# Optimization experiments

Hardware: AMD Instinct MI355X
Metric: run time of the kernel (lower is better)

Reference implementation:

```python
import jax, jax.numpy as jnp
import numpy as np

B, A, C, M, E = 8, 100000, 8, 128, 32
ALPHA, GAMMA = 0.25, 2.0


def setup_inputs() -> dict:
    key = jax.random.key(0)
    k1, k2, k3, k4, k5, k6, k7 = jax.random.split(key, 7)
    classifications = jax.random.uniform(k1, (B, A, C), dtype=jnp.float32)
    regressions = jax.random.normal(k2, (B, A, 8), dtype=jnp.float32)
    embeddings = jax.random.normal(k3, (B, A, E), dtype=jnp.float32)
    # anchors: random centers on a 1920x1080 image, reasonable w/h -> x1,y1,x2,y2
    cx = jax.random.uniform(k4, (A,), minval=0.0, maxval=1920.0)
    cy = jax.random.uniform(jax.random.fold_in(k4, 1), (A,), minval=0.0, maxval=1080.0)
    w = jax.random.uniform(jax.random.fold_in(k4, 2), (A,), minval=16.0, maxval=256.0)
    h = jax.random.uniform(jax.random.fold_in(k4, 3), (A,), minval=16.0, maxval=256.0)
    anchors = jnp.stack([cx - 0.5 * w, cy - 0.5 * h, cx + 0.5 * w, cy + 0.5 * h], axis=1)[None].astype(jnp.float32)
    # annotations: 16 coords = jittered 3D-box corner projections around a random box,
    # col 16 = object id, col 17 = class label in [0, C)
    bcx = jax.random.uniform(k5, (B, M, 1), minval=100.0, maxval=1820.0)
    bcy = jax.random.uniform(jax.random.fold_in(k5, 1), (B, M, 1), minval=100.0, maxval=980.0)
    bw = jax.random.uniform(jax.random.fold_in(k5, 2), (B, M, 1), minval=30.0, maxval=300.0)
    bh = jax.random.uniform(jax.random.fold_in(k5, 3), (B, M, 1), minval=30.0, maxval=300.0)
    jit = jax.random.uniform(k6, (B, M, 16), minval=-0.4, maxval=0.4)
    sx = jnp.array([-1, -1, 1, 1, -1, -1, 1, 1], jnp.float32)
    sy = jnp.array([-1, 1, -1, 1, -1, 1, -1, 1], jnp.float32)
    xs = bcx + 0.5 * bw * (sx + jit[..., 0:16:2])
    ys = bcy + 0.5 * bh * (sy + jit[..., 1:16:2])
    coords = jnp.stack([xs, ys], axis=-1).reshape(B, M, 16)
    ids = jax.random.randint(k7, (B, M, 1), 0, 1000).astype(jnp.float32)
    cls_lab = jax.random.randint(jax.random.fold_in(k7, 1), (B, M, 1), 0, C).astype(jnp.float32)
    annotations = jnp.concatenate([coords, ids, cls_lab], axis=-1)
    return {
        "classifications": classifications,
        "regressions": regressions,
        "anchors": anchors,
        "annotations": annotations,
        "embeddings": embeddings,
    }


def calc_iou(a, b):
    # a: [A,4], b: [M,4] in x1,y1,x2,y2 -> [A,M]
    area = (b[:, 2] - b[:, 0]) * (b[:, 3] - b[:, 1])
    iw = jnp.minimum(a[:, 2:3], b[None, :, 2]) - jnp.maximum(a[:, 0:1], b[None, :, 0])
    ih = jnp.minimum(a[:, 3:4], b[None, :, 3]) - jnp.maximum(a[:, 1:2], b[None, :, 1])
    iw = jnp.clip(iw, 0.0)
    ih = jnp.clip(ih, 0.0)
    ua = ((a[:, 2] - a[:, 0]) * (a[:, 3] - a[:, 1]))[:, None] + area[None, :] - iw * ih
    return iw * ih / jnp.clip(ua, 1e-8)


_S2 = jnp.array([-1, -1, 1, 1, -1, -1, 1, 1], jnp.float32)
_S4 = jnp.array([-1, 1, -1, 1, -1, 1, -1, 1], jnp.float32)
_S6 = jnp.array([1, 1, 1, 1, -1, -1, -1, -1], jnp.float32)


def _per_image(cls, reg, ann, anchor):
    # cls [A,C], reg [A,8], ann [M,18], anchor [A,4]
    aw = anchor[:, 2] - anchor[:, 0]
    ah = anchor[:, 3] - anchor[:, 1]
    acx = anchor[:, 0] + 0.5 * aw
    acy = anchor[:, 1] + 0.5 * ah
    cls = jnp.clip(cls, 1e-4, 1.0 - 1e-4)
    valid = ann[:, -1] >= 0.0  # [M]; annotations with class -1 are padding
    xs, ys = ann[:, 0:16:2], ann[:, 1:16:2]
    box2d = jnp.stack([xs.min(1), ys.min(1), xs.max(1), ys.max(1)], axis=1)  # [M,4]
    iou = jnp.where(valid[None, :], calc_iou(anchor, box2d), -1.0)  # [A,M]
    iou_max = iou.max(1)
    assigned = ann[iou.argmax(1)]  # [A,18]
    pos = iou_max >= 0.5
    neg = iou_max < 0.4
    num_pos = jnp.maximum(pos.sum().astype(cls.dtype), 1.0)

    onehot = jax.nn.one_hot(assigned[:, -1].astype(jnp.int32), cls.shape[1], dtype=cls.dtype)
    targets = jnp.where(pos[:, None], onehot, jnp.where(neg[:, None], 0.0, -1.0))
    alpha_f = jnp.where(targets == 1.0, ALPHA, 1.0 - ALPHA)
    focal_w = alpha_f * jnp.where(targets == 1.0, 1.0 - cls, cls) ** GAMMA
    bce = -(targets * jnp.log(cls) + (1.0 - targets) * jnp.log(1.0 - cls))
    cls_loss = jnp.where(targets != -1.0, focal_w * bce, 0.0).sum() / num_pos

    t = assigned[:, :16]

    def vp(rx, ry, tx, ty):
        denom = jnp.sqrt(rx * rx + ry * ry) * jnp.sqrt(tx * tx + ty * ty)
        return 1.0 - (rx * tx + ry * ty) / jnp.maximum(denom, 1e-8)

    vp1 = vp(reg[:, 2], reg[:, 3],
             (t[:, 4] + t[:, 6] + t[:, 12] + t[:, 14] - (t[:, 0] + t[:, 2] + t[:, 8] + t[:, 10])) / 4.0,
             (t[:, 5] + t[:, 7] + t[:, 13] + t[:, 15] - (t[:, 1] + t[:, 3] + t[:, 9] + t[:, 11])) / 4.0)
    vp2 = vp(reg[:, 4], reg[:, 5],
             (t[:, 2] + t[:, 6] + t[:, 10] + t[:, 14] - (t[:, 0] + t[:, 4] + t[:, 8] + t[:, 12])) / 4.0,
             (t[:, 3] + t[:, 7] + t[:, 11] + t[:, 15] - (t[:, 1] + t[:, 5] + t[:, 9] + t[:, 13])) / 4.0)
    vp3 = vp(reg[:, 6], reg[:, 7],
             (t[:, 0] + t[:, 2] + t[:, 4] + t[:, 6] - (t[:, 8] + t[:, 10] + t[:, 12] + t[:, 14])) / 4.0,
             (t[:, 1] + t[:, 3] + t[:, 5] + t[:, 7] - (t[:, 9] + t[:, 11] + t[:, 13] + t[:, 15])) / 4.0)
    vp_all = (vp1 + vp2 + vp3) / 3.0
    vp_loss = (vp_all * pos).sum() / num_pos

    # corner predictions from (ctr_x, ctr_y, v1, v2, v3) offsets: [A,8] x-coords, [A,8] y-coords
    px = reg[:, 0:1] + reg[:, 2:3] * _S2 + reg[:, 4:5] * _S4 + reg[:, 6:7] * _S6
    py = reg[:, 1:2] + reg[:, 3:4] * _S2 + reg[:, 5:6] * _S4 + reg[:, 7:8] * _S6
    tx = (t[:, 0:16:2] - acx[:, None]) / aw[:, None]
    ty = (t[:, 1:16:2] - acy[:, None]) / ah[:, None]
    diff = jnp.concatenate([jnp.abs(px - tx), jnp.abs(py - ty)], axis=1)  # [A,16]
    sl1 = jnp.where(diff <= 1.0 / 9.0, 0.5 * 9.0 * diff * diff, diff - 0.5 / 9.0)
    reg_loss = (sl1.mean(1) * pos).sum() / num_pos
    return cls_loss, reg_loss, vp_loss


def reference(classifications, regressions, anchors, annotations, embeddings):
    anchor = anchors[0]
    cls_l, reg_l, vp_l = jax.vmap(_per_image, in_axes=(0, 0, 0, None))(
        classifications, regressions, annotations, anchor)
    return jnp.stack([cls_l.mean(), reg_l.mean(), vp_l.mean()])


if __name__ == "__main__":
    print(reference(**setup_inputs()))
```

## Files before the change

kernel.cpp:

```cpp
#include <hip/hip_runtime.h>

namespace {

constexpr int B_N = 8;
constexpr int A_N = 100000;
constexpr int M_N = 128;
constexpr int BLOCK = 256;
constexpr int NBLK_S = (A_N + BLOCK - 1) / BLOCK;
constexpr int GX = 16, GY = 9, NC = GX * GY;
constexpr float CELL = 120.0f;
constexpr float MARGIN = 128.0f;
constexpr int CPC = 4;
constexpr int NCH = NC * CPC;

constexpr size_t OFF_BOX  = 0;
constexpr size_t OFF_MASK = OFF_BOX + (size_t)B_N * M_N * 8 * 4;
constexpr size_t OFF_HIST = OFF_MASK + (size_t)B_N * NC * 2 * 8;
constexpr size_t OFF_OFFS = OFF_HIST + (size_t)NBLK_S * NC * 4;
constexpr size_t OFF_CT   = OFF_OFFS + (size_t)NC * NBLK_S * 4;
constexpr size_t OFF_CB   = OFF_CT + NC * 4;
constexpr size_t OFF_SIDX = (OFF_CB + (NC + 1) * 4 + 15) & ~size_t(15);
constexpr size_t OFF_SANC = (OFF_SIDX + (size_t)A_N * 4 + 15) & ~size_t(15);
constexpr size_t OFF_PART = OFF_SANC + (size_t)A_N * 16;

__device__ __forceinline__ int cell_of(const float4& an) {
    const float acx = 0.5f * (an.x + an.z);
    const float acy = 0.5f * (an.y + an.w);
    const int cx = min(GX - 1, max(0, (int)(acx * (1.0f / CELL))));
    const int cy = min(GY - 1, max(0, (int)(acy * (1.0f / CELL))));
    return cy * GX + cx;
}

__global__ void f0_prep_mask(const float* __restrict__ ann_,
                             float* __restrict__ boxbuf,
                             unsigned long long* __restrict__ maskbuf)
{
    const int cell = blockIdx.x, b = blockIdx.y, m = threadIdx.x;
    const float* t = ann_ + ((size_t)b * M_N + m) * 18;
    float minx = t[0], maxx = t[0], miny = t[1], maxy = t[1];
#pragma unroll
    for (int j = 1; j < 8; ++j) {
        const float xj = t[2 * j], yj = t[2 * j + 1];
        minx = fminf(minx, xj); maxx = fmaxf(maxx, xj);
        miny = fminf(miny, yj); maxy = fmaxf(maxy, yj);
    }
    float area = (maxx - minx) * (maxy - miny);
    if (t[17] < 0.0f) {
        minx = 1e30f; miny = 1e30f; maxx = -1e30f; maxy = -1e30f; area = 0.0f;
    }
    if (cell == 0) {
        float* o = boxbuf + ((size_t)b * M_N + m) * 8;
        o[0] = minx; o[1] = miny; o[2] = maxx; o[3] = maxy;
        o[4] = area; o[5] = 0.f;  o[6] = 0.f;  o[7] = 0.f;
    }
    const int cx = cell % GX, cy = cell / GX;
    const float lox = cx * CELL - MARGIN, hix = cx * CELL + CELL + MARGIN;
    const float loy = cy * CELL - MARGIN, hiy = cy * CELL + CELL + MARGIN;
    const bool ok = (minx <= hix) && (maxx >= lox) && (miny <= hiy) && (maxy >= loy);
    const unsigned long long bal = __ballot(ok);
    if ((m & 63) == 0)
        maskbuf[((size_t)b * NC + cell) * 2 + (m >> 6)] = bal;
}

__global__ __launch_bounds__(BLOCK) void s1_hist(
    const float* __restrict__ anchors_, unsigned* __restrict__ hist)
{
    __shared__ unsigned h[NC];
    const int tid = threadIdx.x, blk = blockIdx.x;
    for (int i = tid; i < NC; i += BLOCK) h[i] = 0u;
    __syncthreads();
    const int a = blk * BLOCK + tid;
    if (a < A_N) {
        const float4 an = ((const float4*)anchors_)[a];
        atomicAdd(&h[cell_of(an)], 1u);
    }
    __syncthreads();
    for (int i = tid; i < NC; i += BLOCK) hist[(size_t)blk * NC + i] = h[i];
}

__global__ __launch_bounds__(BLOCK) void s2a_scan(
    const unsigned* __restrict__ hist,
    unsigned* __restrict__ offs,
    unsigned* __restrict__ cellTot)
{
    const int c = blockIdx.x, t = threadIdx.x;
    const int k0 = 2 * t, k1 = 2 * t + 1;
    const unsigned v0 = (k0 < NBLK_S) ? hist[(size_t)k0 * NC + c] : 0u;
    const unsigned v1 = (k1 < NBLK_S) ? hist[(size_t)k1 * NC + c] : 0u;
    const unsigned mysum = v0 + v1;
    __shared__ unsigned s[BLOCK];
    s[t] = mysum;
    __syncthreads();
    for (int off = 1; off < BLOCK; off <<= 1) {
        const unsigned x = (t >= off) ? s[t - off] : 0u;
        __syncthreads();
        s[t] += x;
        __syncthreads();
    }
    const unsigned excl = s[t] - mysum;
    if (k0 < NBLK_S) offs[(size_t)c * NBLK_S + k0] = excl;
    if (k1 < NBLK_S) offs[(size_t)c * NBLK_S + k1] = excl + v0;
    if (t == BLOCK - 1) cellTot[c] = s[BLOCK - 1];
}

__global__ __launch_bounds__(BLOCK) void s3_scatter(
    const float* __restrict__ anchors_,
    const unsigned* __restrict__ offs,
    const unsigned* __restrict__ cellTot,
    unsigned* __restrict__ cellBase,
    unsigned* __restrict__ sidx, float4* __restrict__ sanc)
{
    __shared__ unsigned sscan[BLOCK];
    __shared__ unsigned scb[NC];
    __shared__ unsigned hw[4][NC];
    const int tid = threadIdx.x, blk = blockIdx.x;

    const unsigned v = (tid < NC) ? cellTot[tid] : 0u;
    sscan[tid] = v;
    for (int i = tid; i < 4 * NC; i += BLOCK) (&hw[0][0])[i] = 0u;
    __syncthreads();
    for (int off = 1; off < BLOCK; off <<= 1) {
        const unsigned x = (tid >= off) ? sscan[tid - off] : 0u;
        __syncthreads();
        sscan[tid] += x;
        __syncthreads();
    }
    if (tid < NC) scb[tid] = sscan[tid] - v;
    if (blk == 0) {
        if (tid < NC) cellBase[tid] = sscan[tid] - v;
        if (tid == NC - 1) cellBase[NC] = sscan[tid];
    }

    const int a = blk * BLOCK + tid;
    const bool valid = (a < A_N);
    float4 an = make_float4(0.f, 0.f, 0.f, 0.f);
    int c = -1;
    if (valid) { an = ((const float4*)anchors_)[a]; c = cell_of(an); }
    const int ln = tid & 63, wv = tid >> 6;

    int rank = 0, cnt = 0;
    for (int j = 0; j < 64; ++j) {
        const int cj = __shfl(c, j);
        const bool same = (cj == c);
        rank += (same && (j < ln));
        cnt  += same;
    }
    if (valid && rank == 0) hw[wv][c] = (unsigned)cnt;
    __syncthreads();
    if (valid) {
        unsigned r = (unsigned)rank;
        for (int w = 0; w < wv; ++w) r += hw[w][c];
        const unsigned d = scb[c] + offs[(size_t)c * NBLK_S + blk] + r;
        sidx[d] = (unsigned)a;
        sanc[d] = an;
    }
}

__global__ __launch_bounds__(BLOCK) void ka2(
    const float* __restrict__ cls_,
    const float* __restrict__ reg_,
    const float* __restrict__ ann_,
    const float* __restrict__ boxbuf,
    const unsigned* __restrict__ maskbuf,
    const unsigned* __restrict__ cellBase,
    const unsigned* __restrict__ sidx,
    const float4* __restrict__ sanc,
    float* __restrict__ partials)
{
    const int cc = blockIdx.x / CPC, chunk = blockIdx.x % CPC;
    const int b = blockIdx.y, tid = threadIdx.x;
    const int base = (int)cellBase[cc];
    const int n    = (int)cellBase[cc + 1] - base;

    if (chunk * BLOCK >= n) {
        if (tid == 0) {
            float* o = partials + ((size_t)b * NCH + blockIdx.x) * 4;
            o[0] = 0.f; o[1] = 0.f; o[2] = 0.f; o[3] = 0.f;
        }
        return;
    }

    __shared__ float s_x1[M_N], s_y1[M_N], s_x2[M_N], s_y2[M_N], s_nb[M_N];
    __shared__ int   s_id[M_N];
    __shared__ unsigned s_mask[4], s_pre[4];
    __shared__ int s_Kv;

    if (tid < 4) s_mask[tid] = maskbuf[((size_t)b * NC + cc) * 4 + tid];
    __syncthreads();
    if (tid == 0) {
        unsigned p = 0;
#pragma unroll
        for (int w = 0; w < 4; ++w) { s_pre[w] = p; p += __popc(s_mask[w]); }
        s_Kv = (int)p;
    }
    __syncthreads();
    if (tid < M_N) {
        const unsigned w = s_mask[tid >> 5];
        if ((w >> (tid & 31)) & 1u) {
            const int r = (int)(s_pre[tid >> 5] + __popc(w & ((1u << (tid & 31)) - 1u)));
            const float* rec = boxbuf + ((size_t)b * M_N + tid) * 8;
            s_x1[r] = rec[0]; s_y1[r] = rec[1];
            s_x2[r] = rec[2]; s_y2[r] = rec[3];
            s_nb[r] = -rec[4];
            s_id[r] = tid;
        }
    }
    __syncthreads();
    const int K = s_Kv;

    const int i0  = chunk * BLOCK + tid;
    const bool inb = (i0 < n);
    const int gi  = base + (inb ? i0 : 0);
    const float4 an = sanc[gi];
    const int a = (int)sidx[gi];

    const float* cp = cls_ + ((size_t)b * A_N + a) * 8;
    const float4 cA = ((const float4*)cp)[0];
    const float4 cB = ((const float4*)cp)[1];

    const float aarea = (an.z - an.x) * (an.w - an.y);
    float m1 = -3e38f, m2 = -3e38f;
    float bn = 0.f, bs = 1.f;
    int   kb = 0;

    for (int m = 0; m < K; ++m) {
        const float x1 = s_x1[m], y1 = s_y1[m];
        const float x2 = s_x2[m], y2 = s_y2[m];
        const float nb = s_nb[m];
        const float iw = fminf(an.z, x2) - fmaxf(an.x, x1);
        const float ih = fminf(an.w, y2) - fmaxf(an.y, y1);
        const float in_ = fmaxf(iw, 0.f) * fmaxf(ih, 0.f);
        m1 = fmaxf(m1, __builtin_fmaf(3.0f, in_, nb));
        m2 = fmaxf(m2, __builtin_fmaf(3.5f, in_, nb));
        const float s = aarea - nb;
        const bool  u = (in_ * bs > bn * s);
        bn = u ? in_ : bn;
        bs = u ? s   : bs;
        kb = u ? m   : kb;
    }

    const bool pos = inb && (m1 >= aarea);
    const bool nonign = pos || (m2 < aarea);

    float clsS = 0.f, regS = 0.f, vpS = 0.f, posC = 0.f;
    const float pv[8] = {cA.x, cA.y, cA.z, cA.w, cB.x, cB.y, cB.z, cB.w};
    {
        float s = 0.f;
#pragma unroll
        for (int c = 0; c < 8; ++c) {
            const float p = fminf(fmaxf(pv[c], 1e-4f), 1.0f - 1e-4f);
            s += 0.75f * p * p * (-__logf(1.0f - p));
        }
        clsS = (inb && nonign) ? s : 0.f;
    }

    if (pos) {
        posC = 1.0f;
        const float* t = ann_ + ((size_t)b * M_N + s_id[kb]) * 18;
        float tt[16];
#pragma unroll
        for (int j = 0; j < 16; ++j) tt[j] = t[j];
        const int kc = (int)t[17];

        float pkc = 0.5f;
#pragma unroll
        for (int c = 0; c < 8; ++c)
            if (c == kc) pkc = fminf(fmaxf(pv[c], 1e-4f), 1.0f - 1e-4f);
        const float negkc   = 0.75f * pkc * pkc * (-__logf(1.0f - pkc));
        const float posterm = 0.25f * (1.0f - pkc) * (1.0f - pkc) * (-__logf(pkc));
        clsS += posterm - negkc;

        const float aw = an.z - an.x;
        const float ah = an.w - an.y;
        const float* rp = reg_ + ((size_t)b * A_N + a) * 8;
        const float4 r0 = ((const float4*)rp)[0];
        const float4 r1 = ((const float4*)rp)[1];

        auto vp = [](float rx, float ry, float tx, float ty) {
            const float denom = sqrtf(rx * rx + ry * ry) * sqrtf(tx * tx + ty * ty);
            return 1.0f - (rx * tx + ry * ty) / fmaxf(denom, 1e-8f);
        };
        const float vp1 = vp(r0.z, r0.w,
            (tt[4] + tt[6] + tt[12] + tt[14] - (tt[0] + tt[2] + tt[8] + tt[10])) * 0.25f,
            (tt[5] + tt[7] + tt[13] + tt[15] - (tt[1] + tt[3] + tt[9] + tt[11])) * 0.25f);
        const float vp2 = vp(r1.x, r1.y,
            (tt[2] + tt[6] + tt[10] + tt[14] - (tt[0] + tt[4] + tt[8] + tt[12])) * 0.25f,
            (tt[3] + tt[7] + tt[11] + tt[15] - (tt[1] + tt[5] + tt[9] + tt[13])) * 0.25f);
        const float vp3 = vp(r1.z, r1.w,
            (tt[0] + tt[2] + tt[4] + tt[6] - (tt[8] + tt[10] + tt[12] + tt[14])) * 0.25f,
            (tt[1] + tt[3] + tt[5] + tt[7] - (tt[9] + tt[11] + tt[13] + tt[15])) * 0.25f);
        vpS = (vp1 + vp2 + vp3) * (1.0f / 3.0f);

        const float s2v[8] = {-1, -1, 1, 1, -1, -1, 1, 1};
        const float s4v[8] = {-1, 1, -1, 1, -1, 1, -1, 1};
        const float s6v[8] = {1, 1, 1, 1, -1, -1, -1, -1};
        const float acx2 = an.x + 0.5f * aw;
        const float acy2 = an.y + 0.5f * ah;
        float ssum = 0.f;
#pragma unroll
        for (int j = 0; j < 8; ++j) {
            const float px = r0.x + r0.z * s2v[j] + r1.x * s4v[j] + r1.z * s6v[j];
            const float py = r0.y + r0.w * s2v[j] + r1.y * s4v[j] + r1.w * s6v[j];
            const float tx = (tt[2 * j]     - acx2) / aw;
            const float ty = (tt[2 * j + 1] - acy2) / ah;
            const float dx = fabsf(px - tx);
            const float dy = fabsf(py - ty);
            ssum += (dx <= (1.0f / 9.0f)) ? 4.5f * dx * dx : dx - (0.5f / 9.0f);
            ssum += (dy <= (1.0f / 9.0f)) ? 4.5f * dy * dy : dy - (0.5f / 9.0f);
        }
        regS = ssum * (1.0f / 16.0f);
    }

#pragma unroll
    for (int off = 32; off; off >>= 1) {
        clsS += __shfl_down(clsS, off);
        regS += __shfl_down(regS, off);
        vpS  += __shfl_down(vpS, off);
        posC += __shfl_down(posC, off);
    }
    __shared__ float s_red[4][4];
    const int wv = tid >> 6, ln = tid & 63;
    if (ln == 0) {
        s_red[wv][0] = clsS; s_red[wv][1] = regS;
        s_red[wv][2] = vpS;  s_red[wv][3] = posC;
    }
    __syncthreads();
    if (tid == 0) {
        float C = 0, R = 0, V = 0, P = 0;
        for (int w2 = 0; w2 < 4; ++w2) {
            C += s_red[w2][0]; R += s_red[w2][1];
            V += s_red[w2][2]; P += s_red[w2][3];
        }
        float* out = partials + ((size_t)b * NCH + blockIdx.x) * 4;
        out[0] = C; out[1] = R; out[2] = V; out[3] = P;
    }
}

__global__ __launch_bounds__(BLOCK) void kc_final(
    const float* __restrict__ partials,
    float* __restrict__ out)
{
    const int tid = threadIdx.x;
    __shared__ float s[4][4];
    __shared__ float accum[3];
    if (tid == 0) { accum[0] = 0.f; accum[1] = 0.f; accum[2] = 0.f; }

    for (int b = 0; b < B_N; ++b) {
        float c = 0.f, r = 0.f, v = 0.f, p = 0.f;
        for (int i = tid; i < NCH; i += BLOCK) {
            const float* q = partials + ((size_t)b * NCH + i) * 4;
            c += q[0]; r += q[1]; v += q[2]; p += q[3];
        }
#pragma unroll
        for (int off = 32; off; off >>= 1) {
            c += __shfl_down(c, off); r += __shfl_down(r, off);
            v += __shfl_down(v, off); p += __shfl_down(p, off);
        }
        const int wv = tid >> 6, ln = tid & 63;
        if (ln == 0) { s[wv][0] = c; s[wv][1] = r; s[wv][2] = v; s[wv][3] = p; }
        __syncthreads();
        if (tid == 0) {
            float C = 0, R = 0, V = 0, P = 0;
            for (int w = 0; w < 4; ++w) {
                C += s[w][0]; R += s[w][1]; V += s[w][2]; P += s[w][3];
            }
            const float np_ = fmaxf(P, 1.0f);
            accum[0] += C / np_; accum[1] += R / np_; accum[2] += V / np_;
        }
        __syncthreads();
    }
    if (tid == 0) {
        out[0] = accum[0] * 0.125f;
        out[1] = accum[1] * 0.125f;
        out[2] = accum[2] * 0.125f;
    }
}

}

extern "C" void kernel_launch(void* const* d_in, const int* in_sizes, int n_in,
                              void* d_out, int out_size, void* d_ws, size_t ws_size,
                              hipStream_t stream)
{
    const float* cls_    = (const float*)d_in[0];
    const float* reg_    = (const float*)d_in[1];
    const float* anchors = (const float*)d_in[2];
    const float* ann     = (const float*)d_in[3];

    char* ws = (char*)d_ws;
    float*              boxbuf  = (float*)(ws + OFF_BOX);
    unsigned long long* maskbuf = (unsigned long long*)(ws + OFF_MASK);
    unsigned*           hist    = (unsigned*)(ws + OFF_HIST);
    unsigned*           offs    = (unsigned*)(ws + OFF_OFFS);
    unsigned*           cellTot = (unsigned*)(ws + OFF_CT);
    unsigned*           cellBase= (unsigned*)(ws + OFF_CB);
    unsigned*           sidxp   = (unsigned*)(ws + OFF_SIDX);
    float4*             sancp   = (float4*)(ws + OFF_SANC);
    float*              partials= (float*)(ws + OFF_PART);

    f0_prep_mask<<<dim3(NC, B_N), dim3(M_N), 0, stream>>>(ann, boxbuf, maskbuf);
    s1_hist<<<dim3(NBLK_S), dim3(BLOCK), 0, stream>>>(anchors, hist);
    s2a_scan<<<dim3(NC), dim3(BLOCK), 0, stream>>>(hist, offs, cellTot);
    s3_scatter<<<dim3(NBLK_S), dim3(BLOCK), 0, stream>>>(anchors, offs, cellTot,
                                                         cellBase, sidxp, sancp);
    ka2<<<dim3(NCH, B_N), dim3(BLOCK), 0, stream>>>(
        cls_, reg_, ann, boxbuf, (const unsigned*)maskbuf, cellBase,
        sidxp, sancp, partials);
    kc_final<<<dim3(1), dim3(BLOCK), 0, stream>>>(partials, (float*)d_out);
}
```

Baseline: 65.33 us.

## Precompute per-anchor negative focal sums in histogram pass and fold box prep into ka2

The per-anchor, per-image negative focal-loss sum over 8 classes now runs in the histogram kernel. That kernel reads the classification array coalesced in original anchor order and writes one float per anchor per image. The main kernel reads that single float through the sorted index instead of gathering 32 bytes of class probabilities per anchor. It then loads only the one positive-class probability when an anchor is positive. The separate annotation box/mask prep kernel is removed: each ka2 block computes the box bounds and cell-overlap ballot itself. This trades an extra write and read of a B*A float buffer and redundant per-block annotation work for fewer scattered loads and one fewer launch.

```diff
diff --git a/kernel.cpp b/kernel.cpp
--- a/kernel.cpp
+++ b/kernel.cpp
@@ -13,15 +13,14 @@
 constexpr int CPC = 4;
 constexpr int NCH = NC * CPC;
 
-constexpr size_t OFF_BOX  = 0;
-constexpr size_t OFF_MASK = OFF_BOX + (size_t)B_N * M_N * 8 * 4;
-constexpr size_t OFF_HIST = OFF_MASK + (size_t)B_N * NC * 2 * 8;
+constexpr size_t OFF_HIST = 0;
 constexpr size_t OFF_OFFS = OFF_HIST + (size_t)NBLK_S * NC * 4;
 constexpr size_t OFF_CT   = OFF_OFFS + (size_t)NC * NBLK_S * 4;
 constexpr size_t OFF_CB   = OFF_CT + NC * 4;
 constexpr size_t OFF_SIDX = (OFF_CB + (NC + 1) * 4 + 15) & ~size_t(15);
 constexpr size_t OFF_SANC = (OFF_SIDX + (size_t)A_N * 4 + 15) & ~size_t(15);
-constexpr size_t OFF_PART = OFF_SANC + (size_t)A_N * 16;
+constexpr size_t OFF_SNEG = OFF_SANC + (size_t)A_N * 16;
+constexpr size_t OFF_PART = OFF_SNEG + (size_t)B_N * A_N * 4;
 
 __device__ __forceinline__ int cell_of(const float4& an) {
     const float acx = 0.5f * (an.x + an.z);
@@ -31,39 +30,11 @@
     return cy * GX + cx;
 }
 
-__global__ void f0_prep_mask(const float* __restrict__ ann_,
-                             float* __restrict__ boxbuf,
-                             unsigned long long* __restrict__ maskbuf)
-{
-    const int cell = blockIdx.x, b = blockIdx.y, m = threadIdx.x;
-    const float* t = ann_ + ((size_t)b * M_N + m) * 18;
-    float minx = t[0], maxx = t[0], miny = t[1], maxy = t[1];
-#pragma unroll
-    for (int j = 1; j < 8; ++j) {
-        const float xj = t[2 * j], yj = t[2 * j + 1];
-        minx = fminf(minx, xj); maxx = fmaxf(maxx, xj);
-        miny = fminf(miny, yj); maxy = fmaxf(maxy, yj);
-    }
-    float area = (maxx - minx) * (maxy - miny);
-    if (t[17] < 0.0f) {
-        minx = 1e30f; miny = 1e30f; maxx = -1e30f; maxy = -1e30f; area = 0.0f;
-    }
-    if (cell == 0) {
-        float* o = boxbuf + ((size_t)b * M_N + m) * 8;
-        o[0] = minx; o[1] = miny; o[2] = maxx; o[3] = maxy;
-        o[4] = area; o[5] = 0.f;  o[6] = 0.f;  o[7] = 0.f;
-    }
-    const int cx = cell % GX, cy = cell / GX;
-    const float lox = cx * CELL - MARGIN, hix = cx * CELL + CELL + MARGIN;
-    const float loy = cy * CELL - MARGIN, hiy = cy * CELL + CELL + MARGIN;
-    const bool ok = (minx <= hix) && (maxx >= lox) && (miny <= hiy) && (maxy >= loy);
-    const unsigned long long bal = __ballot(ok);
-    if ((m & 63) == 0)
-        maskbuf[((size_t)b * NC + cell) * 2 + (m >> 6)] = bal;
-}
-
-__global__ __launch_bounds__(BLOCK) void s1_hist(
-    const float* __restrict__ anchors_, unsigned* __restrict__ hist)
+__global__ __launch_bounds__(BLOCK) void s1k(
+    const float* __restrict__ anchors_,
+    const float* __restrict__ cls_,
+    unsigned* __restrict__ hist,
+    float* __restrict__ sneg_)
 {
     __shared__ unsigned h[NC];
     const int tid = threadIdx.x, blk = blockIdx.x;
@@ -73,6 +44,20 @@
     if (a < A_N) {
         const float4 an = ((const float4*)anchors_)[a];
         atomicAdd(&h[cell_of(an)], 1u);
+#pragma unroll
+        for (int b = 0; b < B_N; ++b) {
+            const float* cp = cls_ + ((size_t)b * A_N + a) * 8;
+            const float4 cA = ((const float4*)cp)[0];
+            const float4 cB = ((const float4*)cp)[1];
+            const float pv[8] = {cA.x, cA.y, cA.z, cA.w, cB.x, cB.y, cB.z, cB.w};
+            float s = 0.f;
+#pragma unroll
+            for (int c = 0; c < 8; ++c) {
+                const float p = fminf(fmaxf(pv[c], 1e-4f), 1.0f - 1e-4f);
+                s += 0.75f * p * p * (-__logf(1.0f - p));
+            }
+            sneg_[(size_t)b * A_N + a] = s;
+        }
     }
     __syncthreads();
     for (int i = tid; i < NC; i += BLOCK) hist[(size_t)blk * NC + i] = h[i];
@@ -160,8 +145,7 @@
     const float* __restrict__ cls_,
     const float* __restrict__ reg_,
     const float* __restrict__ ann_,
-    const float* __restrict__ boxbuf,
-    const unsigned* __restrict__ maskbuf,
+    const float* __restrict__ sneg_,
     const unsigned* __restrict__ cellBase,
     const unsigned* __restrict__ sidx,
     const float4* __restrict__ sanc,
@@ -182,28 +166,45 @@
 
     __shared__ float s_x1[M_N], s_y1[M_N], s_x2[M_N], s_y2[M_N], s_nb[M_N];
     __shared__ int   s_id[M_N];
-    __shared__ unsigned s_mask[4], s_pre[4];
+    __shared__ unsigned long long s_w[2];
+    __shared__ unsigned s_pre[2];
     __shared__ int s_Kv;
 
-    if (tid < 4) s_mask[tid] = maskbuf[((size_t)b * NC + cc) * 4 + tid];
+    const int ccx = cc % GX, ccy = cc / GX;
+    const float lox = ccx * CELL - MARGIN, hix = ccx * CELL + CELL + MARGIN;
+    const float loy = ccy * CELL - MARGIN, hiy = ccy * CELL + CELL + MARGIN;
+    bool ok = false;
+    float minx = 0.f, miny = 0.f, maxx = 0.f, maxy = 0.f, area = 0.f;
+    if (tid < M_N) {
+        const float* t = ann_ + ((size_t)b * M_N + tid) * 18;
+        minx = t[0]; maxx = t[0]; miny = t[1]; maxy = t[1];
+#pragma unroll
+        for (int j = 1; j < 8; ++j) {
+            const float x = t[2 * j], y = t[2 * j + 1];
+            minx = fminf(minx, x); maxx = fmaxf(maxx, x);
+            miny = fminf(miny, y); maxy = fmaxf(maxy, y);
+        }
+        area = (maxx - minx) * (maxy - miny);
+        ok = (t[17] >= 0.0f) && (minx <= hix) && (maxx >= lox) &&
+             (miny <= hiy) && (maxy >= loy);
+    }
+    const unsigned long long bw = __ballot(ok);
+    if (tid < 128 && (tid & 63) == 0) s_w[tid >> 6] = bw;
     __syncthreads();
     if (tid == 0) {
-        unsigned p = 0;
-#pragma unroll
-        for (int w = 0; w < 4; ++w) { s_pre[w] = p; p += __popc(s_mask[w]); }
-        s_Kv = (int)p;
-    }
-    __syncthreads();
-    if (tid < M_N) {
-        const unsigned w = s_mask[tid >> 5];
-        if ((w >> (tid & 31)) & 1u) {
-            const int r = (int)(s_pre[tid >> 5] + __popc(w & ((1u << (tid & 31)) - 1u)));
-            const float* rec = boxbuf + ((size_t)b * M_N + tid) * 8;
-            s_x1[r] = rec[0]; s_y1[r] = rec[1];
-            s_x2[r] = rec[2]; s_y2[r] = rec[3];
-            s_nb[r] = -rec[4];
-            s_id[r] = tid;
-        }
+        const unsigned p0 = (unsigned)__popcll(s_w[0]);
+        s_pre[0] = 0u; s_pre[1] = p0;
+        s_Kv = (int)(p0 + (unsigned)__popcll(s_w[1]));
+    }
+    __syncthreads();
+    if (ok) {
+        const int wq = tid >> 6;
+        const int r = (int)(s_pre[wq] +
+            (unsigned)__popcll(s_w[wq] & ((1ull << (tid & 63)) - 1ull)));
+        s_x1[r] = minx; s_y1[r] = miny;
+        s_x2[r] = maxx; s_y2[r] = maxy;
+        s_nb[r] = -area;
+        s_id[r] = tid;
     }
     __syncthreads();
     const int K = s_Kv;
@@ -213,10 +214,7 @@
     const int gi  = base + (inb ? i0 : 0);
     const float4 an = sanc[gi];
     const int a = (int)sidx[gi];
-
-    const float* cp = cls_ + ((size_t)b * A_N + a) * 8;
-    const float4 cA = ((const float4*)cp)[0];
-    const float4 cB = ((const float4*)cp)[1];
+    const float sneg_v = sneg_[(size_t)b * A_N + a];
 
     const float aarea = (an.z - an.x) * (an.w - an.y);
     float m1 = -3e38f, m2 = -3e38f;
@@ -242,17 +240,8 @@
     const bool pos = inb && (m1 >= aarea);
     const bool nonign = pos || (m2 < aarea);
 
-    float clsS = 0.f, regS = 0.f, vpS = 0.f, posC = 0.f;
-    const float pv[8] = {cA.x, cA.y, cA.z, cA.w, cB.x, cB.y, cB.z, cB.w};
-    {
-        float s = 0.f;
-#pragma unroll
-        for (int c = 0; c < 8; ++c) {
-            const float p = fminf(fmaxf(pv[c], 1e-4f), 1.0f - 1e-4f);
-            s += 0.75f * p * p * (-__logf(1.0f - p));
-        }
-        clsS = (inb && nonign) ? s : 0.f;
-    }
+    float clsS = (inb && nonign) ? sneg_v : 0.f;
+    float regS = 0.f, vpS = 0.f, posC = 0.f;
 
     if (pos) {
         posC = 1.0f;
@@ -262,10 +251,8 @@
         for (int j = 0; j < 16; ++j) tt[j] = t[j];
         const int kc = (int)t[17];
 
-        float pkc = 0.5f;
-#pragma unroll
-        for (int c = 0; c < 8; ++c)
-            if (c == kc) pkc = fminf(fmaxf(pv[c], 1e-4f), 1.0f - 1e-4f);
+        const float praw = cls_[((size_t)b * A_N + a) * 8 + kc];
+        const float pkc = fminf(fmaxf(praw, 1e-4f), 1.0f - 1e-4f);
         const float negkc   = 0.75f * pkc * pkc * (-__logf(1.0f - pkc));
         const float posterm = 0.25f * (1.0f - pkc) * (1.0f - pkc) * (-__logf(pkc));
         clsS += posterm - negkc;
@@ -388,23 +375,20 @@
     const float* ann     = (const float*)d_in[3];
 
     char* ws = (char*)d_ws;
-    float*              boxbuf  = (float*)(ws + OFF_BOX);
-    unsigned long long* maskbuf = (unsigned long long*)(ws + OFF_MASK);
-    unsigned*           hist    = (unsigned*)(ws + OFF_HIST);
-    unsigned*           offs    = (unsigned*)(ws + OFF_OFFS);
-    unsigned*           cellTot = (unsigned*)(ws + OFF_CT);
-    unsigned*           cellBase= (unsigned*)(ws + OFF_CB);
-    unsigned*           sidxp   = (unsigned*)(ws + OFF_SIDX);
-    float4*             sancp   = (float4*)(ws + OFF_SANC);
-    float*              partials= (float*)(ws + OFF_PART);
-
-    f0_prep_mask<<<dim3(NC, B_N), dim3(M_N), 0, stream>>>(ann, boxbuf, maskbuf);
-    s1_hist<<<dim3(NBLK_S), dim3(BLOCK), 0, stream>>>(anchors, hist);
+    unsigned* hist     = (unsigned*)(ws + OFF_HIST);
+    unsigned* offs     = (unsigned*)(ws + OFF_OFFS);
+    unsigned* cellTot  = (unsigned*)(ws + OFF_CT);
+    unsigned* cellBase = (unsigned*)(ws + OFF_CB);
+    unsigned* sidxp    = (unsigned*)(ws + OFF_SIDX);
+    float4*   sancp    = (float4*)(ws + OFF_SANC);
+    float*    snegp    = (float*)(ws + OFF_SNEG);
+    float*    partials = (float*)(ws + OFF_PART);
+
+    s1k<<<dim3(NBLK_S), dim3(BLOCK), 0, stream>>>(anchors, cls_, hist, snegp);
     s2a_scan<<<dim3(NC), dim3(BLOCK), 0, stream>>>(hist, offs, cellTot);
     s3_scatter<<<dim3(NBLK_S), dim3(BLOCK), 0, stream>>>(anchors, offs, cellTot,
                                                          cellBase, sidxp, sancp);
     ka2<<<dim3(NCH, B_N), dim3(BLOCK), 0, stream>>>(
-        cls_, reg_, ann, boxbuf, (const unsigned*)maskbuf, cellBase,
-        sidxp, sancp, partials);
+        cls_, reg_, ann, snegp, cellBase, sidxp, sancp, partials);
     kc_final<<<dim3(1), dim3(BLOCK), 0, stream>>>(partials, (float*)d_out);
 }
```

After: 63.51 us. 1.03x faster.
